# Kernel optimization log

Hardware: AMD Instinct MI355X
Metric: run time of the kernel (lower is better)

## Reference

```python
import jax, jax.numpy as jnp
import numpy as np

N = 100000   # nodes
E = 1600000  # edges
F = 64       # num_features
H = 64       # hidden_units
C = 10       # num_classes
G = 1000     # graphs in batch
BN_EPS = 1e-5


def setup_inputs() -> dict:
    key = jax.random.key(0)
    ks = jax.random.split(key, 32)
    inp = {
        "x": jax.random.normal(ks[0], (N, F), dtype=jnp.float32),
        "edge_index": jax.random.randint(ks[1], (2, E), 0, N, dtype=jnp.int64),
        "batch": jnp.sort(jax.random.randint(ks[2], (N,), 0, G, dtype=jnp.int64)),
    }
    i = 3
    def w(shape, scale):
        nonlocal i
        a = jax.random.normal(ks[i], shape, dtype=jnp.float32) * scale
        i += 1
        return a
    for l, din in [(0, F), (1, H)]:
        inp[f"c{l}_w1"] = w((din, H), 1.0 / np.sqrt(din))
        inp[f"c{l}_b1"] = jnp.zeros((H,), jnp.float32)
        inp[f"c{l}_g1"] = jnp.ones((H,), jnp.float32)
        inp[f"c{l}_be1"] = jnp.zeros((H,), jnp.float32)
        inp[f"c{l}_w2"] = w((H, H), 1.0 / np.sqrt(H))
        inp[f"c{l}_b2"] = jnp.zeros((H,), jnp.float32)
        inp[f"bn{l}_g"] = jnp.ones((H,), jnp.float32)
        inp[f"bn{l}_b"] = jnp.zeros((H,), jnp.float32)
    for l, din in [(0, F), (1, H), (2, H)]:
        inp[f"l{l}_w"] = w((din, C), 1.0 / np.sqrt(din))
        inp[f"l{l}_b"] = jnp.zeros((C,), jnp.float32)
    return inp


def _bn(h, g, b):
    # BatchNorm1d in training mode: batch statistics over node axis
    m = jnp.mean(h, axis=0)
    v = jnp.var(h, axis=0)
    return g * (h - m) * jax.lax.rsqrt(v + BN_EPS) + b


def _gin_conv(h, src, dst, w1, b1, g1, be1, w2, b2):
    # scatter-add neighbor aggregation: out[dst] += h[src]; eps = 0
    agg = jax.ops.segment_sum(h[src], dst, num_segments=N)
    z = h + agg                      # (1 + eps) * x + sum_j x_j
    z = jax.nn.relu(_bn(z @ w1 + b1, g1, be1))
    return z @ w2 + b2


def reference(x, edge_index, batch,
              c0_w1, c0_b1, c0_g1, c0_be1, c0_w2, c0_b2, bn0_g, bn0_b,
              c1_w1, c1_b1, c1_g1, c1_be1, c1_w2, c1_b2, bn1_g, bn1_b,
              l0_w, l0_b, l1_w, l1_b, l2_w, l2_b):
    src, dst = edge_index[0], edge_index[1]
    h0 = x
    h1 = jax.nn.relu(_bn(_gin_conv(h0, src, dst, c0_w1, c0_b1, c0_g1, c0_be1, c0_w2, c0_b2), bn0_g, bn0_b))
    h2 = jax.nn.relu(_bn(_gin_conv(h1, src, dst, c1_w1, c1_b1, c1_g1, c1_be1, c1_w2, c1_b2), bn1_g, bn1_b))
    # jumping-knowledge readout: per-layer global_add_pool -> Linear -> sum (dropout=0)
    out = jnp.zeros((G, C), dtype=x.dtype)
    for h, w, b in [(h0, l0_w, l0_b), (h1, l1_w, l1_b), (h2, l2_w, l2_b)]:
        pooled = jax.ops.segment_sum(h, batch, num_segments=G)
        out = out + pooled @ w + b
    return out
```

## Files before the change

kernel.cpp:

```cpp
#include <hip/hip_runtime.h>
#include <hip/hip_bf16.h>

#define BN_EPS 1e-5f
#define NBMAX 512
#define CHUNK 4096
#define CAPC  6144

typedef __hip_bfloat16 bf16;
typedef __attribute__((ext_vector_type(8))) short short8;
typedef __attribute__((ext_vector_type(4))) float f32x4;

__device__ __forceinline__ float b2f(bf16 v) { return __bfloat162float(v); }
__device__ __forceinline__ bf16 f2b(float v) { return __float2bfloat16(v); }
__device__ __forceinline__ float bl(unsigned u) { return __uint_as_float(u << 16); }
__device__ __forceinline__ float bh(unsigned u) { return __uint_as_float(u & 0xffff0000u); }
__device__ __forceinline__ unsigned pack2(float x, float y) {
    union { bf16 b[2]; unsigned u; } p;
    p.b[0] = f2b(x); p.b[1] = f2b(y);
    return p.u;
}
__device__ __forceinline__ float bs2f(short s) {
    return __uint_as_float(((unsigned)(unsigned short)s) << 16);
}
__device__ __forceinline__ short f2bs(float v) {
    bf16 b = f2b(v);
    return *reinterpret_cast<short*>(&b);
}

__global__ __launch_bounds__(1024) void init_k(int* __restrict__ btot, int nbp1)
{
    int t = threadIdx.x;
    if (t < nbp1) btot[t] = 0;
}


__global__ __launch_bounds__(256) void bincount_k(
    const int* __restrict__ dst, int* __restrict__ btot, int E, int NB)
{
    __shared__ int h[NBMAX];
    for (int i = threadIdx.x; i < NB; i += 256) h[i] = 0;
    __syncthreads();
    const int base = blockIdx.x * CHUNK;
    const int lim = min(CHUNK, E - base);
    for (int i = threadIdx.x; i < lim; i += 256)
        atomicAdd(&h[dst[base + i] >> 8], 1);
    __syncthreads();
    for (int i = threadIdx.x; i < NB; i += 256)
        if (h[i]) atomicAdd(&btot[i], h[i]);
}

__global__ __launch_bounds__(256) void bucketscan_k(
    const int* __restrict__ btot, int* __restrict__ bbase,
    int* __restrict__ bcur, int* __restrict__ rowptr, int NB, int N, int E)
{
    __shared__ int s[256];
    const int t = threadIdx.x;
    int v0 = (2 * t     < NB) ? btot[2 * t]     : 0;
    int v1 = (2 * t + 1 < NB) ? btot[2 * t + 1] : 0;
    s[t] = v0 + v1;
    __syncthreads();
    for (int off = 1; off < 256; off <<= 1) {
        int a = (t >= off) ? s[t - off] : 0;
        __syncthreads();
        s[t] += a;
        __syncthreads();
    }
    int excl = s[t] - (v0 + v1);
    if (2 * t < NB)     { bbase[2 * t] = excl;          bcur[2 * t] = excl; }
    if (2 * t + 1 < NB) { bbase[2 * t + 1] = excl + v0; bcur[2 * t + 1] = excl + v0; }
    if (t == 0) { bbase[NB] = E; rowptr[N] = E; }
}

__global__ __launch_bounds__(256) void binscatter_k(
    const int* __restrict__ src, const int* __restrict__ dst,
    int* __restrict__ bcur, int* __restrict__ tmp, int E, int NB)
{
    __shared__ int hist[NBMAX];
    __shared__ int loff[NBMAX];
    __shared__ int gb[NBMAX];
    __shared__ int lcur[NBMAX];
    __shared__ int staged[CHUNK];
    __shared__ unsigned short sb[CHUNK];
    __shared__ int ssc[256];
    const int t = threadIdx.x;
    for (int i = t; i < NB; i += 256) { hist[i] = 0; lcur[i] = 0; }
    __syncthreads();
    const int base = blockIdx.x * CHUNK;
    const int lim = min(CHUNK, E - base);
    int myb[16], myw[16];
    int cnt = 0;
    for (int i = t; i < lim; i += 256) {
        int d = dst[base + i];
        int s_ = src[base + i];
        int b = d >> 8;
        myb[cnt] = b;
        myw[cnt] = (s_ << 8) | (d & 255);
        cnt++;
        atomicAdd(&hist[b], 1);
    }
    __syncthreads();
    int v0 = (2 * t     < NB) ? hist[2 * t]     : 0;
    int v1 = (2 * t + 1 < NB) ? hist[2 * t + 1] : 0;
    ssc[t] = v0 + v1;
    __syncthreads();
    for (int off = 1; off < 256; off <<= 1) {
        int a = (t >= off) ? ssc[t - off] : 0;
        __syncthreads();
        ssc[t] += a;
        __syncthreads();
    }
    int excl = ssc[t] - (v0 + v1);
    if (2 * t < NB)     loff[2 * t] = excl;
    if (2 * t + 1 < NB) loff[2 * t + 1] = excl + v0;
    __syncthreads();
    for (int b = t; b < NB; b += 256)
        if (hist[b] > 0) gb[b] = atomicAdd(&bcur[b], hist[b]);
    for (int i = 0; i < cnt; i++) {
        int b = myb[i];
        int p = loff[b] + atomicAdd(&lcur[b], 1);
        staged[p] = myw[i];
        sb[p] = (unsigned short)b;
    }
    __syncthreads();
    for (int i = t; i < lim; i += 256) {
        int b = sb[i];
        tmp[gb[b] + (i - loff[b])] = staged[i];
    }
}

__global__ __launch_bounds__(256) void csr_k(
    const int* __restrict__ bbase, const int* __restrict__ tmp,
    int* __restrict__ rowptr, int* __restrict__ adj, int N)
{
    __shared__ int hist[256], pfx[256], cur[256], ssc[256];
    __shared__ int sadj[CAPC];
    const int b = blockIdx.x, t = threadIdx.x;
    const int lo = bbase[b], hi = bbase[b + 1];
    const int cnt = hi - lo;
    hist[t] = 0; cur[t] = 0;
    __syncthreads();
    for (int i = t; i < cnt; i += 256)
        atomicAdd(&hist[tmp[lo + i] & 255], 1);
    __syncthreads();
    int v = hist[t];
    ssc[t] = v;
    __syncthreads();
    for (int off = 1; off < 256; off <<= 1) {
        int a = (t >= off) ? ssc[t - off] : 0;
        __syncthreads();
        ssc[t] += a;
        __syncthreads();
    }
    pfx[t] = ssc[t] - v;
    const int node = b * 256 + t;
    if (node < N) rowptr[node] = lo + pfx[t];
    __syncthreads();
    if (cnt <= CAPC) {
        for (int i = t; i < cnt; i += 256) {
            int w = tmp[lo + i];
            int d = w & 255;
            int p = pfx[d] + atomicAdd(&cur[d], 1);
            sadj[p] = w >> 8;
        }
        __syncthreads();
        for (int i = t; i < cnt; i += 256) adj[lo + i] = sadj[i];
    } else {
        for (int i = t; i < cnt; i += 256) {
            int w = tmp[lo + i];
            int d = w & 255;
            int p = pfx[d] + atomicAdd(&cur[d], 1);
            adj[lo + p] = w >> 8;
        }
    }
}

template<int AFFINE>
__global__ __launch_bounds__(256) void aggregate_k(
    const bf16* __restrict__ h, const int* __restrict__ rowptr,
    const int* __restrict__ adj, bf16* __restrict__ z, int N,
    const float* __restrict__ sc, const float* __restrict__ sh)
{
    const int lane = threadIdx.x & 31;
    const int n = blockIdx.x * 8 + (threadIdx.x >> 5);
    float sc0 = 0.f, sc1 = 0.f, sh0 = 0.f, sh1 = 0.f;
    if (AFFINE) {
        const int f0 = lane * 2;
        sc0 = sc[f0]; sc1 = sc[f0 + 1];
        sh0 = sh[f0]; sh1 = sh[f0 + 1];
    }
    if (n >= N) return;
    const unsigned* hp = (const unsigned*)h;
    const int b = rowptr[n], e = rowptr[n + 1];

    unsigned u = hp[(size_t)n * 32 + lane];
    float a0 = bl(u), a1 = bh(u);
    if (AFFINE) {
        a0 = fmaxf(fmaf(a0, sc0, sh0), 0.f);
        a1 = fmaxf(fmaf(a1, sc1, sh1), 0.f);
    }
    float s0 = a0, s1 = a1;

    int i = b;
    for (; i + 16 <= e; i += 16) {
        int m[16];
        #pragma unroll
        for (int k = 0; k < 16; k++) m[k] = adj[i + k];
        unsigned w[16];
        #pragma unroll
        for (int k = 0; k < 16; k++) w[k] = hp[(size_t)m[k] * 32 + lane];
        #pragma unroll
        for (int k = 0; k < 16; k++) {
            float p0 = bl(w[k]), p1 = bh(w[k]);
            if (AFFINE) {
                p0 = fmaxf(fmaf(p0, sc0, sh0), 0.f);
                p1 = fmaxf(fmaf(p1, sc1, sh1), 0.f);
            }
            s0 += p0; s1 += p1;
        }
    }
    for (; i + 4 <= e; i += 4) {
        int m[4];
        #pragma unroll
        for (int k = 0; k < 4; k++) m[k] = adj[i + k];
        #pragma unroll
        for (int k = 0; k < 4; k++) {
            unsigned w = hp[(size_t)m[k] * 32 + lane];
            float p0 = bl(w), p1 = bh(w);
            if (AFFINE) {
                p0 = fmaxf(fmaf(p0, sc0, sh0), 0.f);
                p1 = fmaxf(fmaf(p1, sc1, sh1), 0.f);
            }
            s0 += p0; s1 += p1;
        }
    }
    for (; i < e; i++) {
        unsigned w = hp[(size_t)adj[i] * 32 + lane];
        float p0 = bl(w), p1 = bh(w);
        if (AFFINE) {
            p0 = fmaxf(fmaf(p0, sc0, sh0), 0.f);
            p1 = fmaxf(fmaf(p1, sc1, sh1), 0.f);
        }
        s0 += p0; s1 += p1;
    }
    ((unsigned*)z)[(size_t)n * 32 + lane] = pack2(s0, s1);
}

template<int MODE>
__global__ __launch_bounds__(256) void gemm64_k(
    const bf16* __restrict__ A,
    const float* __restrict__ scin, const float* __restrict__ shin,
    const float* __restrict__ W, const float* __restrict__ bias,
    bf16* __restrict__ out, float* __restrict__ pstat, int nrows)
{
    __shared__ bf16 sWt[64][72];
    __shared__ float sSc[64], sSh[64], sB[64];
    __shared__ float sredS[64][17], sredQ[64][17];
    const int tid = threadIdx.x;

    if (tid < 64) {
        sB[tid] = bias[tid];
        if (MODE == 1) { sSc[tid] = scin[tid]; sSh[tid] = shin[tid]; }
    }
    for (int i = tid; i < 4096; i += 256) {
        int k = i >> 6, n = i & 63;
        sWt[n][k] = f2b(W[i]);
    }
    __syncthreads();

    const int wave = tid >> 6, lane = tid & 63;
    const int quad = lane >> 4, l16 = lane & 15;
    const int row0 = blockIdx.x * 128 + wave * 32;

    short8 a[2][2];
    #pragma unroll
    for (int rt = 0; rt < 2; rt++) {
        int r = row0 + rt * 16 + l16;
        int rr = min(r, nrows - 1);
        const bf16* arow = A + (size_t)rr * 64;
        a[rt][0] = *(const short8*)(arow + quad * 8);
        a[rt][1] = *(const short8*)(arow + 32 + quad * 8);
        if (MODE == 1) {
            #pragma unroll
            for (int j = 0; j < 8; j++) {
                int f0 = quad * 8 + j;
                a[rt][0][j] = f2bs(fmaxf(fmaf(bs2f(a[rt][0][j]), sSc[f0], sSh[f0]), 0.f));
                int f1 = 32 + f0;
                a[rt][1][j] = f2bs(fmaxf(fmaf(bs2f(a[rt][1][j]), sSc[f1], sSh[f1]), 0.f));
            }
        }
    }

    float psS[4], psQ[4];
    #pragma unroll
    for (int t = 0; t < 4; t++) { psS[t] = 0.f; psQ[t] = 0.f; }

    #pragma unroll
    for (int t = 0; t < 4; t++) {
        const int n = t * 16 + l16;
        short8 b0 = *(const short8*)&sWt[n][quad * 8];
        short8 b1 = *(const short8*)&sWt[n][32 + quad * 8];
        const float bn_ = sB[n];
        #pragma unroll
        for (int rt = 0; rt < 2; rt++) {
            f32x4 acc = {0.f, 0.f, 0.f, 0.f};
            acc = __builtin_amdgcn_mfma_f32_16x16x32_bf16(a[rt][0], b0, acc, 0, 0, 0);
            acc = __builtin_amdgcn_mfma_f32_16x16x32_bf16(a[rt][1], b1, acc, 0, 0, 0);
            #pragma unroll
            for (int reg = 0; reg < 4; reg++) {
                int gr = row0 + rt * 16 + quad * 4 + reg;
                if (gr < nrows) {
                    float v = acc[reg] + bn_;
                    out[(size_t)gr * 64 + n] = f2b(v);
                    psS[t] += v;
                    psQ[t] = fmaf(v, v, psQ[t]);
                }
            }
        }
    }

    #pragma unroll
    for (int t = 0; t < 4; t++) {
        sredS[t * 16 + l16][wave * 4 + quad] = psS[t];
        sredQ[t * 16 + l16][wave * 4 + quad] = psQ[t];
    }
    __syncthreads();
    if (tid < 128) {
        const int c = tid & 63;
        const float* p = (tid < 64) ? &sredS[c][0] : &sredQ[c][0];
        float s = 0.f;
        #pragma unroll
        for (int i = 0; i < 16; i++) s += p[i];
        pstat[(size_t)blockIdx.x * 128 + (tid < 64 ? c : 64 + c)] = s;
    }
}

__global__ __launch_bounds__(256) void bn_reduce_k(
    const float* __restrict__ pstat, int nblk,
    const float* __restrict__ g, const float* __restrict__ be, float invN,
    float* __restrict__ sc, float* __restrict__ sh)
{
    const int f = blockIdx.x;
    const int t = threadIdx.x;
    float S = 0.f, Q = 0.f;
    for (int b = t; b < nblk; b += 256) {
        S += pstat[(size_t)b * 128 + f];
        Q += pstat[(size_t)b * 128 + 64 + f];
    }
    __shared__ float rs[256], rq[256];
    rs[t] = S; rq[t] = Q;
    __syncthreads();
    for (int off = 128; off > 0; off >>= 1) {
        if (t < off) { rs[t] += rs[t + off]; rq[t] += rq[t + off]; }
        __syncthreads();
    }
    if (t == 0) {
        float m = rs[0] * invN;
        float v = rq[0] * invN - m * m;
        float s = g[f] * rsqrtf(v + BN_EPS);
        sc[f] = s;
        sh[f] = be[f] - m * s;
    }
}

__global__ __launch_bounds__(256) void cast_k(
    const float* __restrict__ in, bf16* __restrict__ out, int total4)
{
    int i = blockIdx.x * 256 + threadIdx.x;
    if (i >= total4) return;
    float4 v = ((const float4*)in)[i];
    union { ushort4 u; bf16 b[4]; } p;
    p.b[0] = f2b(v.x); p.b[1] = f2b(v.y); p.b[2] = f2b(v.z); p.b[3] = f2b(v.w);
    ((ushort4*)out)[i] = p.u;
}

__global__ __launch_bounds__(256) void pool_readout_k(
    const bf16* __restrict__ xb, const bf16* __restrict__ z0,
    const bf16* __restrict__ z1, const int* __restrict__ batch,
    const float* __restrict__ scA, const float* __restrict__ shA,
    const float* __restrict__ scB, const float* __restrict__ shB,
    const float* __restrict__ w0, const float* __restrict__ b0,
    const float* __restrict__ w1, const float* __restrict__ b1,
    const float* __restrict__ w2, const float* __restrict__ b2,
    float* __restrict__ out, int Nn)
{
    const int g = blockIdx.x;
    int lo = 0, hi = Nn;
    while (lo < hi) { int mid = (lo + hi) >> 1; if (batch[mid] < g) lo = mid + 1; else hi = mid; }
    const int start = lo;
    hi = Nn;
    while (lo < hi) { int mid = (lo + hi) >> 1; if (batch[mid] <= g) lo = mid + 1; else hi = mid; }
    const int end = lo;

    const int f = threadIdx.x & 63;
    const int w = threadIdx.x >> 6;
    const float sA = scA[f], tA = shA[f];
    const float sB = scB[f], tB = shB[f];

    float s0 = 0.f, s1 = 0.f, s2 = 0.f;
    for (int i = start + w; i < end; i += 4) {
        s0 += b2f(xb[(size_t)i * 64 + f]);
        s1 += fmaxf(fmaf(b2f(z0[(size_t)i * 64 + f]), sA, tA), 0.f);
        s2 += fmaxf(fmaf(b2f(z1[(size_t)i * 64 + f]), sB, tB), 0.f);
    }
    __shared__ float p[3][4][64];
    p[0][w][f] = s0; p[1][w][f] = s1; p[2][w][f] = s2;
    __syncthreads();
    if (threadIdx.x < 10) {
        const int c = threadIdx.x;
        float acc = b0[c] + b1[c] + b2[c];
        for (int k = 0; k < 64; k++) {
            float q0 = p[0][0][k] + p[0][1][k] + p[0][2][k] + p[0][3][k];
            float q1 = p[1][0][k] + p[1][1][k] + p[1][2][k] + p[1][3][k];
            float q2 = p[2][0][k] + p[2][1][k] + p[2][2][k] + p[2][3][k];
            acc = fmaf(q0, w0[k * 10 + c], acc);
            acc = fmaf(q1, w1[k * 10 + c], acc);
            acc = fmaf(q2, w2[k * 10 + c], acc);
        }
        out[(size_t)g * 10 + c] = acc;
    }
}

extern "C" void kernel_launch(void* const* d_in, const int* in_sizes, int n_in,
                              void* d_out, int out_size, void* d_ws, size_t ws_size,
                              hipStream_t stream)
{
    const float* x     = (const float*)d_in[0];
    const int*   edge  = (const int*)d_in[1];
    const int*   batch = (const int*)d_in[2];
    const int N = in_sizes[0] / 64;
    const int E = in_sizes[1] / 2;
    const int G = out_size / 10;
    const int* src = edge;
    const int* dst = edge + E;
    const int NB = (N + 255) / 256;

    const float* c_w1[2]  = {(const float*)d_in[3],  (const float*)d_in[11]};
    const float* c_b1[2]  = {(const float*)d_in[4],  (const float*)d_in[12]};
    const float* c_g1[2]  = {(const float*)d_in[5],  (const float*)d_in[13]};
    const float* c_be1[2] = {(const float*)d_in[6],  (const float*)d_in[14]};
    const float* c_w2[2]  = {(const float*)d_in[7],  (const float*)d_in[15]};
    const float* c_b2[2]  = {(const float*)d_in[8],  (const float*)d_in[16]};
    const float* bn_g[2]  = {(const float*)d_in[9],  (const float*)d_in[17]};
    const float* bn_b[2]  = {(const float*)d_in[10], (const float*)d_in[18]};
    const float* lw[3]    = {(const float*)d_in[19], (const float*)d_in[21], (const float*)d_in[23]};
    const float* lb[3]    = {(const float*)d_in[20], (const float*)d_in[22], (const float*)d_in[24]};

    float* out = (float*)d_out;
    const size_t nh = (size_t)N * 64;
    const int PG = (N + 127) / 128;

    bf16*  zb    = (bf16*)d_ws;
    bf16*  wb    = zb + nh;
    bf16*  xb    = wb + nh;
    float* scsh  = (float*)(xb + nh);
    float* pstat = scsh + 512;
    int*   rowptr   = (int*)(pstat + (size_t)PG * 128);
    int*   adj      = rowptr + N + 1;
    int*   tmp      = adj + E;
    int*   btot     = tmp + E;
    int*   bbase    = btot + NB + 1;
    int*   bcur     = bbase + NB + 1;

    float* sc0 = scsh;       float* sh0 = scsh + 64;
    float* scA = scsh + 128; float* shA = scsh + 192;
    float* sc2 = scsh + 256; float* sh2 = scsh + 320;
    float* scB = scsh + 384; float* shB = scsh + 448;

    const float invN = 1.0f / (float)N;
    const int binGrid  = (E + CHUNK - 1) / CHUNK;
    const int aggGrid  = (N + 7) / 8;
    const int ewGrid   = (int)((nh / 4 + 255) / 256);

    init_k<<<1, 1024, 0, stream>>>(btot, NB + 1);
    bincount_k<<<binGrid, 256, 0, stream>>>(dst, btot, E, NB);
    bucketscan_k<<<1, 256, 0, stream>>>(btot, bbase, bcur, rowptr, NB, N, E);
    binscatter_k<<<binGrid, 256, 0, stream>>>(src, dst, bcur, tmp, E, NB);
    csr_k<<<NB, 256, 0, stream>>>(bbase, tmp, rowptr, adj, N);

    cast_k<<<ewGrid, 256, 0, stream>>>(x, xb, (int)(nh / 4));

    aggregate_k<0><<<aggGrid, 256, 0, stream>>>(xb, rowptr, adj, zb, N, nullptr, nullptr);
    gemm64_k<0><<<PG, 256, 0, stream>>>(zb, nullptr, nullptr,
                                        c_w1[0], c_b1[0], zb, pstat, N);
    bn_reduce_k<<<64, 256, 0, stream>>>(pstat, PG, c_g1[0], c_be1[0], invN, sc0, sh0);
    gemm64_k<1><<<PG, 256, 0, stream>>>(zb, sc0, sh0,
                                        c_w2[0], c_b2[0], zb, pstat, N);
    bn_reduce_k<<<64, 256, 0, stream>>>(pstat, PG, bn_g[0], bn_b[0], invN, scA, shA);

    aggregate_k<1><<<aggGrid, 256, 0, stream>>>(zb, rowptr, adj, wb, N, scA, shA);
    gemm64_k<0><<<PG, 256, 0, stream>>>(wb, nullptr, nullptr,
                                        c_w1[1], c_b1[1], wb, pstat, N);
    bn_reduce_k<<<64, 256, 0, stream>>>(pstat, PG, c_g1[1], c_be1[1], invN, sc2, sh2);
    gemm64_k<1><<<PG, 256, 0, stream>>>(wb, sc2, sh2,
                                        c_w2[1], c_b2[1], wb, pstat, N);
    bn_reduce_k<<<64, 256, 0, stream>>>(pstat, PG, bn_g[1], bn_b[1], invN, scB, shB);

    pool_readout_k<<<G, 256, 0, stream>>>(xb, zb, wb, batch,
                                          scA, shA, scB, shB,
                                          lw[0], lb[0], lw[1], lb[1], lw[2], lb[2],
                                          out, N);
}
```

Measured before the change: 331.1 us.

## Fuse neighbor aggregation with first GIN linear layer; merge init into cast

Neighbor aggregation and the first 64x64 GEMM of each GIN layer now run in one kernel. Each 512-thread block aggregates 128 nodes into shared memory, then runs MFMA on them directly and writes the pre-BN activations and partial BN statistics. This removes a global write and re-read of the aggregated tensor and one launch per layer. The bucket-count zeroing is also folded into the bf16 cast kernel to drop another launch. The trade-offs are higher shared memory use per block, a sync between the gather and GEMM phases, and fewer resident blocks for the latency-bound gather.

```diff
diff --git a/kernel.cpp b/kernel.cpp
--- a/kernel.cpp
+++ b/kernel.cpp
@@ -27,10 +27,19 @@
     return *reinterpret_cast<short*>(&b);
 }
 
-__global__ __launch_bounds__(1024) void init_k(int* __restrict__ btot, int nbp1)
-{
-    int t = threadIdx.x;
-    if (t < nbp1) btot[t] = 0;
+__global__ __launch_bounds__(256) void initcast_k(
+    const float* __restrict__ in, bf16* __restrict__ out, int total4,
+    int* __restrict__ btot, int nbp1)
+{
+    if (blockIdx.x == 0) {
+        for (int i = threadIdx.x; i < nbp1; i += 256) btot[i] = 0;
+    }
+    int i = blockIdx.x * 256 + threadIdx.x;
+    if (i >= total4) return;
+    float4 v = ((const float4*)in)[i];
+    union { ushort4 u; bf16 b[4]; } p;
+    p.b[0] = f2b(v.x); p.b[1] = f2b(v.y); p.b[2] = f2b(v.z); p.b[3] = f2b(v.w);
+    ((ushort4*)out)[i] = p.u;
 }
 
 
@@ -175,56 +184,83 @@
 }
 
 template<int AFFINE>
-__global__ __launch_bounds__(256) void aggregate_k(
+__global__ __launch_bounds__(512, 6) void agg_gemm_k(
     const bf16* __restrict__ h, const int* __restrict__ rowptr,
-    const int* __restrict__ adj, bf16* __restrict__ z, int N,
-    const float* __restrict__ sc, const float* __restrict__ sh)
-{
-    const int lane = threadIdx.x & 31;
-    const int n = blockIdx.x * 8 + (threadIdx.x >> 5);
+    const int* __restrict__ adj,
+    const float* __restrict__ sc, const float* __restrict__ sh,
+    const float* __restrict__ W, const float* __restrict__ bias,
+    bf16* __restrict__ tout, float* __restrict__ pstat, int N)
+{
+    __shared__ unsigned zt[128][36];
+    __shared__ bf16 sWt[64][72];
+    __shared__ float sB[64];
+    __shared__ float sredS[64][33], sredQ[64][33];
+    const int tid = threadIdx.x;
+
+    if (tid < 64) sB[tid] = bias[tid];
+    for (int i = tid; i < 4096; i += 512) {
+        int k = i >> 6, n = i & 63;
+        sWt[n][k] = f2b(W[i]);
+    }
+
+    const int lane32 = tid & 31;
+    const int hw = tid >> 5;
     float sc0 = 0.f, sc1 = 0.f, sh0 = 0.f, sh1 = 0.f;
     if (AFFINE) {
-        const int f0 = lane * 2;
+        const int f0 = lane32 * 2;
         sc0 = sc[f0]; sc1 = sc[f0 + 1];
         sh0 = sh[f0]; sh1 = sh[f0 + 1];
     }
-    if (n >= N) return;
     const unsigned* hp = (const unsigned*)h;
-    const int b = rowptr[n], e = rowptr[n + 1];
-
-    unsigned u = hp[(size_t)n * 32 + lane];
-    float a0 = bl(u), a1 = bh(u);
-    if (AFFINE) {
-        a0 = fmaxf(fmaf(a0, sc0, sh0), 0.f);
-        a1 = fmaxf(fmaf(a1, sc1, sh1), 0.f);
-    }
-    float s0 = a0, s1 = a1;
-
-    int i = b;
-    for (; i + 16 <= e; i += 16) {
-        int m[16];
-        #pragma unroll
-        for (int k = 0; k < 16; k++) m[k] = adj[i + k];
-        unsigned w[16];
-        #pragma unroll
-        for (int k = 0; k < 16; k++) w[k] = hp[(size_t)m[k] * 32 + lane];
-        #pragma unroll
-        for (int k = 0; k < 16; k++) {
-            float p0 = bl(w[k]), p1 = bh(w[k]);
-            if (AFFINE) {
-                p0 = fmaxf(fmaf(p0, sc0, sh0), 0.f);
-                p1 = fmaxf(fmaf(p1, sc1, sh1), 0.f);
+
+    #pragma unroll 1
+    for (int it = 0; it < 8; it++) {
+        const int local = it * 16 + hw;
+        const int n = blockIdx.x * 128 + local;
+        if (n >= N) { zt[local][lane32] = 0u; continue; }
+        const int b = rowptr[n], e = rowptr[n + 1];
+        unsigned u = hp[(size_t)n * 32 + lane32];
+        float a0 = bl(u), a1 = bh(u);
+        if (AFFINE) {
+            a0 = fmaxf(fmaf(a0, sc0, sh0), 0.f);
+            a1 = fmaxf(fmaf(a1, sc1, sh1), 0.f);
+        }
+        float s0 = a0, s1 = a1;
+        int i = b;
+        for (; i + 16 <= e; i += 16) {
+            int m[16];
+            #pragma unroll
+            for (int k = 0; k < 16; k++) m[k] = adj[i + k];
+            unsigned w[16];
+            #pragma unroll
+            for (int k = 0; k < 16; k++) w[k] = hp[(size_t)m[k] * 32 + lane32];
+            #pragma unroll
+            for (int k = 0; k < 16; k++) {
+                float p0 = bl(w[k]), p1 = bh(w[k]);
+                if (AFFINE) {
+                    p0 = fmaxf(fmaf(p0, sc0, sh0), 0.f);
+                    p1 = fmaxf(fmaf(p1, sc1, sh1), 0.f);
+                }
+                s0 += p0; s1 += p1;
             }
-            s0 += p0; s1 += p1;
-        }
-    }
-    for (; i + 4 <= e; i += 4) {
-        int m[4];
-        #pragma unroll
-        for (int k = 0; k < 4; k++) m[k] = adj[i + k];
-        #pragma unroll
-        for (int k = 0; k < 4; k++) {
-            unsigned w = hp[(size_t)m[k] * 32 + lane];
+        }
+        for (; i + 4 <= e; i += 4) {
+            int m[4];
+            #pragma unroll
+            for (int k = 0; k < 4; k++) m[k] = adj[i + k];
+            #pragma unroll
+            for (int k = 0; k < 4; k++) {
+                unsigned w = hp[(size_t)m[k] * 32 + lane32];
+                float p0 = bl(w), p1 = bh(w);
+                if (AFFINE) {
+                    p0 = fmaxf(fmaf(p0, sc0, sh0), 0.f);
+                    p1 = fmaxf(fmaf(p1, sc1, sh1), 0.f);
+                }
+                s0 += p0; s1 += p1;
+            }
+        }
+        for (; i < e; i++) {
+            unsigned w = hp[(size_t)adj[i] * 32 + lane32];
             float p0 = bl(w), p1 = bh(w);
             if (AFFINE) {
                 p0 = fmaxf(fmaf(p0, sc0, sh0), 0.f);
@@ -232,20 +268,58 @@
             }
             s0 += p0; s1 += p1;
         }
-    }
-    for (; i < e; i++) {
-        unsigned w = hp[(size_t)adj[i] * 32 + lane];
-        float p0 = bl(w), p1 = bh(w);
-        if (AFFINE) {
-            p0 = fmaxf(fmaf(p0, sc0, sh0), 0.f);
-            p1 = fmaxf(fmaf(p1, sc1, sh1), 0.f);
-        }
-        s0 += p0; s1 += p1;
-    }
-    ((unsigned*)z)[(size_t)n * 32 + lane] = pack2(s0, s1);
-}
-
-template<int MODE>
+        zt[local][lane32] = pack2(s0, s1);
+    }
+    __syncthreads();
+
+    const int wave = tid >> 6, lane = tid & 63;
+    const int quad = lane >> 4, l16 = lane & 15;
+    const int rloc = wave * 16 + l16;
+
+    short8 a0 = *(const short8*)&zt[rloc][quad * 4];
+    short8 a1 = *(const short8*)&zt[rloc][16 + quad * 4];
+
+    float psS[4], psQ[4];
+    #pragma unroll
+    for (int t = 0; t < 4; t++) { psS[t] = 0.f; psQ[t] = 0.f; }
+
+    #pragma unroll
+    for (int t = 0; t < 4; t++) {
+        const int n = t * 16 + l16;
+        short8 b0 = *(const short8*)&sWt[n][quad * 8];
+        short8 b1 = *(const short8*)&sWt[n][32 + quad * 8];
+        f32x4 acc = {0.f, 0.f, 0.f, 0.f};
+        acc = __builtin_amdgcn_mfma_f32_16x16x32_bf16(a0, b0, acc, 0, 0, 0);
+        acc = __builtin_amdgcn_mfma_f32_16x16x32_bf16(a1, b1, acc, 0, 0, 0);
+        const float bn_ = sB[n];
+        #pragma unroll
+        for (int reg = 0; reg < 4; reg++) {
+            int gr = blockIdx.x * 128 + wave * 16 + quad * 4 + reg;
+            if (gr < N) {
+                float v = acc[reg] + bn_;
+                tout[(size_t)gr * 64 + n] = f2b(v);
+                psS[t] += v;
+                psQ[t] = fmaf(v, v, psQ[t]);
+            }
+        }
+    }
+
+    #pragma unroll
+    for (int t = 0; t < 4; t++) {
+        sredS[t * 16 + l16][wave * 4 + quad] = psS[t];
+        sredQ[t * 16 + l16][wave * 4 + quad] = psQ[t];
+    }
+    __syncthreads();
+    if (tid < 128) {
+        const int c = tid & 63;
+        const float* p = (tid < 64) ? &sredS[c][0] : &sredQ[c][0];
+        float s = 0.f;
+        #pragma unroll
+        for (int i = 0; i < 32; i++) s += p[i];
+        pstat[(size_t)blockIdx.x * 128 + (tid < 64 ? c : 64 + c)] = s;
+    }
+}
+
 __global__ __launch_bounds__(256) void gemm64_k(
     const bf16* __restrict__ A,
     const float* __restrict__ scin, const float* __restrict__ shin,
@@ -259,7 +333,7 @@
 
     if (tid < 64) {
         sB[tid] = bias[tid];
-        if (MODE == 1) { sSc[tid] = scin[tid]; sSh[tid] = shin[tid]; }
+        sSc[tid] = scin[tid]; sSh[tid] = shin[tid];
     }
     for (int i = tid; i < 4096; i += 256) {
         int k = i >> 6, n = i & 63;
@@ -279,14 +353,12 @@
         const bf16* arow = A + (size_t)rr * 64;
         a[rt][0] = *(const short8*)(arow + quad * 8);
         a[rt][1] = *(const short8*)(arow + 32 + quad * 8);
-        if (MODE == 1) {
-            #pragma unroll
-            for (int j = 0; j < 8; j++) {
-                int f0 = quad * 8 + j;
-                a[rt][0][j] = f2bs(fmaxf(fmaf(bs2f(a[rt][0][j]), sSc[f0], sSh[f0]), 0.f));
-                int f1 = 32 + f0;
-                a[rt][1][j] = f2bs(fmaxf(fmaf(bs2f(a[rt][1][j]), sSc[f1], sSh[f1]), 0.f));
-            }
+        #pragma unroll
+        for (int j = 0; j < 8; j++) {
+            int f0 = quad * 8 + j;
+            a[rt][0][j] = f2bs(fmaxf(fmaf(bs2f(a[rt][0][j]), sSc[f0], sSh[f0]), 0.f));
+            int f1 = 32 + f0;
+            a[rt][1][j] = f2bs(fmaxf(fmaf(bs2f(a[rt][1][j]), sSc[f1], sSh[f1]), 0.f));
         }
     }
 
@@ -362,17 +434,6 @@
     }
 }
 
-__global__ __launch_bounds__(256) void cast_k(
-    const float* __restrict__ in, bf16* __restrict__ out, int total4)
-{
-    int i = blockIdx.x * 256 + threadIdx.x;
-    if (i >= total4) return;
-    float4 v = ((const float4*)in)[i];
-    union { ushort4 u; bf16 b[4]; } p;
-    p.b[0] = f2b(v.x); p.b[1] = f2b(v.y); p.b[2] = f2b(v.z); p.b[3] = f2b(v.w);
-    ((ushort4*)out)[i] = p.u;
-}
-
 __global__ __launch_bounds__(256) void pool_readout_k(
     const bf16* __restrict__ xb, const bf16* __restrict__ z0,
     const bf16* __restrict__ z1, const int* __restrict__ batch,
@@ -468,31 +529,24 @@
 
     const float invN = 1.0f / (float)N;
     const int binGrid  = (E + CHUNK - 1) / CHUNK;
-    const int aggGrid  = (N + 7) / 8;
     const int ewGrid   = (int)((nh / 4 + 255) / 256);
 
-    init_k<<<1, 1024, 0, stream>>>(btot, NB + 1);
+    initcast_k<<<ewGrid, 256, 0, stream>>>(x, xb, (int)(nh / 4), btot, NB + 1);
     bincount_k<<<binGrid, 256, 0, stream>>>(dst, btot, E, NB);
     bucketscan_k<<<1, 256, 0, stream>>>(btot, bbase, bcur, rowptr, NB, N, E);
     binscatter_k<<<binGrid, 256, 0, stream>>>(src, dst, bcur, tmp, E, NB);
     csr_k<<<NB, 256, 0, stream>>>(bbase, tmp, rowptr, adj, N);
 
-    cast_k<<<ewGrid, 256, 0, stream>>>(x, xb, (int)(nh / 4));
-
-    aggregate_k<0><<<aggGrid, 256, 0, stream>>>(xb, rowptr, adj, zb, N, nullptr, nullptr);
-    gemm64_k<0><<<PG, 256, 0, stream>>>(zb, nullptr, nullptr,
-                                        c_w1[0], c_b1[0], zb, pstat, N);
+    agg_gemm_k<0><<<PG, 512, 0, stream>>>(xb, rowptr, adj, nullptr, nullptr,
+                                          c_w1[0], c_b1[0], zb, pstat, N);
     bn_reduce_k<<<64, 256, 0, stream>>>(pstat, PG, c_g1[0], c_be1[0], invN, sc0, sh0);
-    gemm64_k<1><<<PG, 256, 0, stream>>>(zb, sc0, sh0,
-                                        c_w2[0], c_b2[0], zb, pstat, N);
+    gemm64_k<<<PG, 256, 0, stream>>>(zb, sc0, sh0, c_w2[0], c_b2[0], zb, pstat, N);
     bn_reduce_k<<<64, 256, 0, stream>>>(pstat, PG, bn_g[0], bn_b[0], invN, scA, shA);
 
-    aggregate_k<1><<<aggGrid, 256, 0, stream>>>(zb, rowptr, adj, wb, N, scA, shA);
-    gemm64_k<0><<<PG, 256, 0, stream>>>(wb, nullptr, nullptr,
-                                        c_w1[1], c_b1[1], wb, pstat, N);
+    agg_gemm_k<1><<<PG, 512, 0, stream>>>(zb, rowptr, adj, scA, shA,
+                                          c_w1[1], c_b1[1], wb, pstat, N);
     bn_reduce_k<<<64, 256, 0, stream>>>(pstat, PG, c_g1[1], c_be1[1], invN, sc2, sh2);
-    gemm64_k<1><<<PG, 256, 0, stream>>>(wb, sc2, sh2,
-                                        c_w2[1], c_b2[1], wb, pstat, N);
+    gemm64_k<<<PG, 256, 0, stream>>>(wb, sc2, sh2, c_w2[1], c_b2[1], wb, pstat, N);
     bn_reduce_k<<<64, 256, 0, stream>>>(pstat, PG, bn_g[1], bn_b[1], invN, scB, shB);
 
     pool_readout_k<<<G, 256, 0, stream>>>(xb, zb, wb, batch,
```

After: 376.2 us. 13.6% more time.
